# Optimization experiments

Hardware: AMD Instinct MI355X
Metric: run time of the kernel (lower is better)

## Reference

```python
import jax, jax.numpy as jnp
import numpy as np

D_MODEL = 1024
NUM_HEADS = 16
DK = D_MODEL // NUM_HEADS


def setup_inputs() -> dict:
    key = jax.random.key(0)
    ks = jax.random.split(key, 9)
    s = 1.0 / np.sqrt(D_MODEL)
    x = jax.random.normal(ks[0], (4, 2048, D_MODEL), dtype=jnp.float32)
    Wq = jax.random.uniform(ks[1], (D_MODEL, D_MODEL), jnp.float32, -s, s)
    bq = jax.random.uniform(ks[2], (D_MODEL,), jnp.float32, -s, s)
    Wk = jax.random.uniform(ks[3], (D_MODEL, D_MODEL), jnp.float32, -s, s)
    bk = jax.random.uniform(ks[4], (D_MODEL,), jnp.float32, -s, s)
    Wv = jax.random.uniform(ks[5], (D_MODEL, D_MODEL), jnp.float32, -s, s)
    bv = jax.random.uniform(ks[6], (D_MODEL,), jnp.float32, -s, s)
    Wo = jax.random.uniform(ks[7], (D_MODEL, D_MODEL), jnp.float32, -s, s)
    bo = jax.random.uniform(ks[8], (D_MODEL,), jnp.float32, -s, s)
    return {"x": x, "Wq": Wq, "bq": bq, "Wk": Wk, "bk": bk,
            "Wv": Wv, "bv": bv, "Wo": Wo, "bo": bo}


def reference(x, Wq, bq, Wk, bk, Wv, bv, Wo, bo):
    B, S, _ = x.shape
    H, dk = NUM_HEADS, DK
    # QKV projections (nn.Linear: x @ W.T + b), split into heads -> [B,H,S,dk]
    q = (x @ Wq.T + bq).reshape(B, S, H, dk).transpose(0, 2, 1, 3)
    k = (x @ Wk.T + bk).reshape(B, S, H, dk).transpose(0, 2, 1, 3)
    v = (x @ Wv.T + bv).reshape(B, S, H, dk).transpose(0, 2, 1, 3)
    scores = jnp.einsum('bhqd,bhkd->bhqk', q, k) / jnp.sqrt(jnp.asarray(dk, x.dtype))
    causal = jnp.triu(jnp.ones((S, S), dtype=bool), k=1)  # True above diagonal
    scores = jnp.where(causal[None, None], -jnp.inf, scores)
    attn = jax.nn.softmax(scores, axis=-1)  # dropout p=0.0 -> identity
    out = jnp.einsum('bhqk,bhkd->bhqd', attn, v)
    out = out.transpose(0, 2, 1, 3).reshape(B, S, H * dk)
    return out @ Wo.T + bo
```

## Files before the change

kernel.cpp:

```cpp
#include <hip/hip_runtime.h>
#include <stdint.h>


#define D_MODEL 1024
#define NHEAD   16
#define DK      64
#define BATCH   4
#define SEQ     2048
#define MTOT    (BATCH*SEQ)

typedef unsigned short u16;
typedef unsigned int   u32;
typedef __bf16    bf16x8  __attribute__((ext_vector_type(8)));
typedef float     floatx4 __attribute__((ext_vector_type(4)));
typedef __fp16    fp16x2  __attribute__((ext_vector_type(2)));
typedef _Float16  half4_t __attribute__((ext_vector_type(4)));
typedef _Float16  half8_t __attribute__((ext_vector_type(8)));

__device__ __forceinline__ u16 f2bf(float f){
  union { float f; u32 u; } c; c.f = f;
  u32 x = c.u;
  x += 0x7fffu + ((x >> 16) & 1u);
  return (u16)(x >> 16);
}
__device__ __forceinline__ u32 pkh(float a, float b){
  union { fp16x2 h; u32 u; } c; c.h = __builtin_amdgcn_cvt_pkrtz(a, b); return c.u;
}
__device__ __forceinline__ uint4 pk8(const float* __restrict__ p){
  uint4 a = *(const uint4*)p;
  uint4 b = *(const uint4*)(p + 4);
  uint4 r;
  r.x = __builtin_amdgcn_perm(a.y, a.x, 0x07060302);
  r.y = __builtin_amdgcn_perm(a.w, a.z, 0x07060302);
  r.z = __builtin_amdgcn_perm(b.y, b.x, 0x07060302);
  r.w = __builtin_amdgcn_perm(b.w, b.z, 0x07060302);
  return r;
}
__device__ __forceinline__ void gload16(const void* g, void* l){
  __builtin_amdgcn_global_load_lds(
      (const __attribute__((address_space(1))) u32*)g,
      (__attribute__((address_space(3))) u32*)l, 16, 0, 0);
}

__global__ __launch_bounds__(256)
void to_bf16(const float* __restrict__ s, u16* __restrict__ d)
{
  const size_t i = ((size_t)blockIdx.x * 256 + threadIdx.x) * 8;
  *(uint4*)(d + i) = pk8(s + i);
}

template<int MODE>
__global__ __launch_bounds__(128, 2)
void gemm_bt(const u16* __restrict__ A, const float* __restrict__ W,
             const float* __restrict__ bias, void* __restrict__ outv,
             float scale)
{
  __shared__ __align__(16) u16 As[128*32];
  __shared__ __align__(16) u16 Bs[64*32];

  const int t    = threadIdx.x;
  const int m0   = blockIdx.x * 128;
  const int n0   = blockIdx.y * 64;
  const int wid  = t >> 6, lane = t & 63;
  const int wr   = wid;
  const int quad = lane >> 4, l15 = lane & 15;

  const int rS = t >> 2;
  const int kS = (t & 3) * 8;

  floatx4 acc[4][4] = {};

  for (int k0 = 0; k0 < D_MODEL; k0 += 32) {
    __syncthreads();
    gload16(A + (size_t)(m0 + rS      )*D_MODEL + k0 + kS, (char*)As + t*16);
    gload16(A + (size_t)(m0 + rS + 32 )*D_MODEL + k0 + kS, (char*)As + 2048 + t*16);
    gload16(A + (size_t)(m0 + rS + 64 )*D_MODEL + k0 + kS, (char*)As + 4096 + t*16);
    gload16(A + (size_t)(m0 + rS + 96 )*D_MODEL + k0 + kS, (char*)As + 6144 + t*16);
    *(uint4*)&Bs[t*8]        = pk8(W + (size_t)(n0 + rS     )*D_MODEL + k0 + kS);
    *(uint4*)&Bs[t*8 + 1024] = pk8(W + (size_t)(n0 + rS + 32)*D_MODEL + k0 + kS);
    __syncthreads();

    bf16x8 af[4], bf[4];
#pragma unroll
    for (int i = 0; i < 4; ++i) {
      af[i] = *(const bf16x8*)&As[(wr*64 + i*16 + l15)*32 + quad*8];
      bf[i] = *(const bf16x8*)&Bs[(i*16 + l15)*32 + quad*8];
    }
#pragma unroll
    for (int mi = 0; mi < 4; ++mi)
#pragma unroll
      for (int nj = 0; nj < 4; ++nj) {
        if (MODE == 2)
          acc[mi][nj] = __builtin_amdgcn_mfma_f32_16x16x32_bf16(af[mi], bf[nj], acc[mi][nj], 0, 0, 0);
        else
          acc[mi][nj] = __builtin_amdgcn_mfma_f32_16x16x32_bf16(bf[nj], af[mi], acc[mi][nj], 0, 0, 0);
      }
  }

  if (MODE != 2) {
#pragma unroll
    for (int nj = 0; nj < 4; ++nj) {
      const int nb = n0 + nj*16 + quad*4;
      const float4 b4 = *(const float4*)(bias + nb);
#pragma unroll
      for (int mi = 0; mi < 4; ++mi) {
        const int m = m0 + wr*64 + mi*16 + l15;
        floatx4 d = acc[mi][nj];
        const float v0 = (d[0]+b4.x)*scale, v1 = (d[1]+b4.y)*scale;
        const float v2 = (d[2]+b4.z)*scale, v3 = (d[3]+b4.w)*scale;
        if (MODE == 0) {
          float4 s4 = make_float4(v0, v1, v2, v3);
          *(float4*)((float*)outv + (size_t)m*D_MODEL + nb) = s4;
        } else {
          const int b = m >> 11, s = m & 2047, h = nb >> 6, dd = nb & 63;
          u16* dst = (u16*)outv + ((((size_t)b*NHEAD + h)*SEQ + s) << 6) + dd;
          *(uint2*)dst = make_uint2(pkh(v0, v1), pkh(v2, v3));
        }
      }
    }
  } else {
#pragma unroll
    for (int nj = 0; nj < 4; ++nj) {
      const int n  = n0 + nj*16 + l15;
      const float bvv = bias[n];
      const int h = n >> 6, dd = n & 63;
#pragma unroll
      for (int mi = 0; mi < 4; ++mi) {
        const int mb = m0 + wr*64 + mi*16 + quad*4;
        const int b = mb >> 11, s = mb & 2047;
        floatx4 d = acc[mi][nj];
        u16* dst = (u16*)outv + (((size_t)b*NHEAD + h)*DK + dd)*SEQ + s;
        *(uint2*)dst = make_uint2(pkh(d[0]+bvv, d[1]+bvv), pkh(d[2]+bvv, d[3]+bvv));
      }
    }
  }
}

__global__ __launch_bounds__(256, 6)
void attn_fwd(const _Float16* __restrict__ Q, const _Float16* __restrict__ K,
              const _Float16* __restrict__ Vt, u16* __restrict__ O)
{
  __shared__ __align__(16) _Float16 Ks[64][72];
  __shared__ __align__(16) _Float16 Vs[64][72];

  const int bh   = blockIdx.x;
  const int pid  = blockIdx.y;
  const int t    = threadIdx.x;
  const int w    = t >> 6, lane = t & 63;
  const int quad = lane >> 4, l15 = lane & 15;
  const int sr = t >> 3, sc8 = (t & 7) * 8;
  const _Float16* Kb = K  + (size_t)bh * SEQ * DK;
  const _Float16* Vb = Vt + (size_t)bh * DK * SEQ;

#pragma unroll 1
  for (int item = 0; item < 2; ++item) {
    const int rblk = item ? pid : (SEQ/64 - 1 - pid);
    const int r0   = rblk * 64;
    const int qb   = r0 + w * 16;
    const int query = qb + l15;

    half8_t qf[2];
    {
      const _Float16* Qp = Q + ((size_t)bh * SEQ + query) * DK + quad * 8;
      qf[0] = *(const half8_t*)(Qp);
      qf[1] = *(const half8_t*)(Qp + 32);
    }

    float mrow = -1e30f, lpart = 0.f;
    floatx4 o[4] = {};

    const int jend = r0 + 64;
    for (int j0 = 0; j0 < jend; j0 += 64) {
      __syncthreads();
      *(uint4*)&Ks[sr     ][sc8] = *(const uint4*)(Kb + (size_t)(j0 + sr     )*DK + sc8);
      *(uint4*)&Ks[sr + 32][sc8] = *(const uint4*)(Kb + (size_t)(j0 + sr + 32)*DK + sc8);
      *(uint4*)&Vs[sr     ][sc8] = *(const uint4*)(Vb + (size_t)(sr     )*SEQ + j0 + sc8);
      *(uint4*)&Vs[sr + 32][sc8] = *(const uint4*)(Vb + (size_t)(sr + 32)*SEQ + j0 + sc8);
      __syncthreads();
      if (j0 > qb + 15) continue;
      const int ktmax = ((qb + 15 - j0) >> 4) + 1;

      floatx4 st[4];
#pragma unroll
      for (int kt = 0; kt < 4; ++kt) {
        if (kt < ktmax) {
          half8_t a0 = *(const half8_t*)&Ks[kt*16 + l15][quad*8];
          half8_t a1 = *(const half8_t*)&Ks[kt*16 + l15][32 + quad*8];
          floatx4 s = {};
          s = __builtin_amdgcn_mfma_f32_16x16x32_f16(a0, qf[0], s, 0, 0, 0);
          s = __builtin_amdgcn_mfma_f32_16x16x32_f16(a1, qf[1], s, 0, 0, 0);
          st[kt] = s;
        }
      }
#pragma unroll
      for (int kt = 0; kt < 4; ++kt) {
        if (kt < ktmax && j0 + kt*16 + 15 > qb) {
#pragma unroll
          for (int r = 0; r < 4; ++r)
            if (j0 + kt*16 + quad*4 + r > query) st[kt][r] = -1e30f;
        }
      }
      float m0 = -1e30f;
#pragma unroll
      for (int kt = 0; kt < 4; ++kt)
        if (kt < ktmax)
          m0 = fmaxf(m0, fmaxf(fmaxf(st[kt][0], st[kt][1]), fmaxf(st[kt][2], st[kt][3])));
      m0 = fmaxf(m0, __shfl_xor(m0, 16));
      m0 = fmaxf(m0, __shfl_xor(m0, 32));
      const float mn    = fmaxf(mrow, m0);
      const float alpha = exp2f(mrow - mn);
      mrow = mn;
      lpart *= alpha;
      half4_t pf[4];
#pragma unroll
      for (int kt = 0; kt < 4; ++kt) {
        if (kt < ktmax) {
          const float p0 = exp2f(st[kt][0] - mn), p1 = exp2f(st[kt][1] - mn);
          const float p2 = exp2f(st[kt][2] - mn), p3 = exp2f(st[kt][3] - mn);
          lpart += (p0 + p1) + (p2 + p3);
          union { half4_t h; uint2 u; } pc;
          pc.u = make_uint2(pkh(p0, p1), pkh(p2, p3));
          pf[kt] = pc.h;
        }
      }
#pragma unroll
      for (int dt = 0; dt < 4; ++dt) {
        o[dt][0] *= alpha; o[dt][1] *= alpha; o[dt][2] *= alpha; o[dt][3] *= alpha;
      }
#pragma unroll
      for (int dt = 0; dt < 4; ++dt)
#pragma unroll
        for (int kt = 0; kt < 4; ++kt) {
          if (kt < ktmax) {
            half4_t vf = *(const half4_t*)&Vs[dt*16 + l15][kt*16 + quad*4];
            o[dt] = __builtin_amdgcn_mfma_f32_16x16x16f16(vf, pf[kt], o[dt], 0, 0, 0);
          }
        }
    }

    float l = lpart;
    l += __shfl_xor(l, 16);
    l += __shfl_xor(l, 32);
    const float inv = 1.0f / l;
    const int b = bh >> 4, h = bh & 15;
    u16* Op = O + ((size_t)(b * SEQ + query)) * D_MODEL + h * DK + quad * 4;
#pragma unroll
    for (int dt = 0; dt < 4; ++dt) {
      u32 lo = ((u32)f2bf(o[dt][1] * inv) << 16) | f2bf(o[dt][0] * inv);
      u32 hi = ((u32)f2bf(o[dt][3] * inv) << 16) | f2bf(o[dt][2] * inv);
      *(uint2*)(Op + dt * 16) = make_uint2(lo, hi);
    }
  }
}

extern "C" void kernel_launch(void* const* d_in, const int* in_sizes, int n_in,
                              void* d_out, int out_size, void* d_ws, size_t ws_size,
                              hipStream_t stream)
{
  const float* x  = (const float*)d_in[0];
  const float* Wq = (const float*)d_in[1];
  const float* bq = (const float*)d_in[2];
  const float* Wk = (const float*)d_in[3];
  const float* bk = (const float*)d_in[4];
  const float* Wv = (const float*)d_in[5];
  const float* bv = (const float*)d_in[6];
  const float* Wo = (const float*)d_in[7];
  const float* bo = (const float*)d_in[8];

  const size_t tsz = (size_t)MTOT * D_MODEL;
  u16* Qw  = (u16*)d_ws;
  u16* Kw  = Qw + tsz;
  u16* Vtw = Kw + tsz;
  u16* S3  = Vtw + tsz;

  to_bf16<<<(MTOT*D_MODEL)/(256*8), 256, 0, stream>>>(x, S3);

  dim3 gg(MTOT/128, D_MODEL/64);
  gemm_bt<1><<<gg, 128, 0, stream>>>(S3, Wq, bq, Qw,  0.18033688f);
  gemm_bt<1><<<gg, 128, 0, stream>>>(S3, Wk, bk, Kw,  1.0f);
  gemm_bt<2><<<gg, 128, 0, stream>>>(S3, Wv, bv, Vtw, 1.0f);

  attn_fwd<<<dim3(BATCH*NHEAD, SEQ/128), 256, 0, stream>>>(
      (const _Float16*)Qw, (const _Float16*)Kw, (const _Float16*)Vtw, S3);

  gemm_bt<0><<<gg, 128, 0, stream>>>(S3, Wo, bo, d_out, 1.0f);
}
```

Measured before the change: 356.6 us.

## Double-buffer LDS tiles in projection GEMM to overlap loads with MFMA

Converts the bf16 GEMM main loop to a double-buffered LDS scheme. The next A tile is issued via global_load_lds and the next W tile is prefetched into registers before the current tile's MFMAs run, so global latency can hide behind compute. The loop now needs one barrier per iteration instead of two. In exchange it uses twice the LDS per block and more registers for the prefetched W values, which may hurt occupancy under launch_bounds(128,2).

```diff
diff --git a/kernel.cpp b/kernel.cpp
--- a/kernel.cpp
+++ b/kernel.cpp
@@ -36,6 +36,14 @@
   r.w = __builtin_amdgcn_perm(b.w, b.z, 0x07060302);
   return r;
 }
+__device__ __forceinline__ uint4 pk8v(uint4 a, uint4 b){
+  uint4 r;
+  r.x = __builtin_amdgcn_perm(a.y, a.x, 0x07060302);
+  r.y = __builtin_amdgcn_perm(a.w, a.z, 0x07060302);
+  r.z = __builtin_amdgcn_perm(b.y, b.x, 0x07060302);
+  r.w = __builtin_amdgcn_perm(b.w, b.z, 0x07060302);
+  return r;
+}
 __device__ __forceinline__ void gload16(const void* g, void* l){
   __builtin_amdgcn_global_load_lds(
       (const __attribute__((address_space(1))) u32*)g,
@@ -55,8 +63,8 @@
              const float* __restrict__ bias, void* __restrict__ outv,
              float scale)
 {
-  __shared__ __align__(16) u16 As[128*32];
-  __shared__ __align__(16) u16 Bs[64*32];
+  __shared__ __align__(16) u16 As[2][128*32];
+  __shared__ __align__(16) u16 Bs[2][64*32];
 
   const int t    = threadIdx.x;
   const int m0   = blockIdx.x * 128;
@@ -68,23 +76,44 @@
   const int rS = t >> 2;
   const int kS = (t & 3) * 8;
 
+  const u16*   Ap  = A + (size_t)(m0 + rS)*D_MODEL + kS;
+  const float* Wp0 = W + (size_t)(n0 + rS)*D_MODEL + kS;
+  const float* Wp1 = Wp0 + (size_t)32*D_MODEL;
+
+  {
+    uint4 w0 = *(const uint4*)(Wp0), w1 = *(const uint4*)(Wp0 + 4);
+    uint4 w2 = *(const uint4*)(Wp1), w3 = *(const uint4*)(Wp1 + 4);
+    gload16(Ap,                (char*)As[0] + t*16);
+    gload16(Ap + 32*D_MODEL,   (char*)As[0] + 2048 + t*16);
+    gload16(Ap + 64*D_MODEL,   (char*)As[0] + 4096 + t*16);
+    gload16(Ap + 96*D_MODEL,   (char*)As[0] + 6144 + t*16);
+    *(uint4*)&Bs[0][t*8]        = pk8v(w0, w1);
+    *(uint4*)&Bs[0][t*8 + 1024] = pk8v(w2, w3);
+  }
+  __syncthreads();
+
   floatx4 acc[4][4] = {};
-
+  int cur = 0;
+
+#pragma unroll 1
   for (int k0 = 0; k0 < D_MODEL; k0 += 32) {
-    __syncthreads();
-    gload16(A + (size_t)(m0 + rS      )*D_MODEL + k0 + kS, (char*)As + t*16);
-    gload16(A + (size_t)(m0 + rS + 32 )*D_MODEL + k0 + kS, (char*)As + 2048 + t*16);
-    gload16(A + (size_t)(m0 + rS + 64 )*D_MODEL + k0 + kS, (char*)As + 4096 + t*16);
-    gload16(A + (size_t)(m0 + rS + 96 )*D_MODEL + k0 + kS, (char*)As + 6144 + t*16);
-    *(uint4*)&Bs[t*8]        = pk8(W + (size_t)(n0 + rS     )*D_MODEL + k0 + kS);
-    *(uint4*)&Bs[t*8 + 1024] = pk8(W + (size_t)(n0 + rS + 32)*D_MODEL + k0 + kS);
-    __syncthreads();
+    const int nxt = k0 + 32;
+    const bool more = nxt < D_MODEL;
+    uint4 w0, w1, w2, w3;
+    if (more) {
+      w0 = *(const uint4*)(Wp0 + nxt); w1 = *(const uint4*)(Wp0 + nxt + 4);
+      w2 = *(const uint4*)(Wp1 + nxt); w3 = *(const uint4*)(Wp1 + nxt + 4);
+      gload16(Ap + nxt,               (char*)As[cur^1] + t*16);
+      gload16(Ap + nxt + 32*D_MODEL,  (char*)As[cur^1] + 2048 + t*16);
+      gload16(Ap + nxt + 64*D_MODEL,  (char*)As[cur^1] + 4096 + t*16);
+      gload16(Ap + nxt + 96*D_MODEL,  (char*)As[cur^1] + 6144 + t*16);
+    }
 
     bf16x8 af[4], bf[4];
 #pragma unroll
     for (int i = 0; i < 4; ++i) {
-      af[i] = *(const bf16x8*)&As[(wr*64 + i*16 + l15)*32 + quad*8];
-      bf[i] = *(const bf16x8*)&Bs[(i*16 + l15)*32 + quad*8];
+      af[i] = *(const bf16x8*)&As[cur][(wr*64 + i*16 + l15)*32 + quad*8];
+      bf[i] = *(const bf16x8*)&Bs[cur][(i*16 + l15)*32 + quad*8];
     }
 #pragma unroll
     for (int mi = 0; mi < 4; ++mi)
@@ -95,6 +124,13 @@
         else
           acc[mi][nj] = __builtin_amdgcn_mfma_f32_16x16x32_bf16(bf[nj], af[mi], acc[mi][nj], 0, 0, 0);
       }
+
+    if (more) {
+      *(uint4*)&Bs[cur^1][t*8]        = pk8v(w0, w1);
+      *(uint4*)&Bs[cur^1][t*8 + 1024] = pk8v(w2, w3);
+    }
+    __syncthreads();
+    cur ^= 1;
   }
 
   if (MODE != 2) {
```

New measurement: 361.0 us. No clear change (+1.2%).
